# Kernel tuning notes

Hardware: AMD Instinct MI355X
Metric: run time of the kernel (lower is better)

## Reference

```python
import jax, jax.numpy as jnp
import numpy as np

B, S, H, NH = 4, 4096, 1024, 16
D = H // NH
SCALE = 1.0 / float(np.sqrt(D))


def setup_inputs() -> dict:
    key = jax.random.key(0)
    ks = jax.random.split(key, 4)
    w = 0.02
    return {
        "hidden_states": jax.random.normal(ks[0], (B, S, H), jnp.float32),
        "attention_mask": jnp.zeros((B, 1, 1, S), jnp.float32),
        "Wq": jax.random.normal(ks[1], (H, H), jnp.float32) * w,
        "bq": jnp.zeros((H,), jnp.float32),
        "Wk": jax.random.normal(ks[2], (H, H), jnp.float32) * w,
        "bk": jnp.zeros((H,), jnp.float32),
        "Wv": jax.random.normal(ks[3], (H, H), jnp.float32) * w,
        "bv": jnp.zeros((H,), jnp.float32),
    }


def reference(hidden_states, attention_mask, Wq, bq, Wk, bk, Wv, bv):
    def heads(x):  # [B,S,H] -> [B,NH,S,D]
        return x.reshape(B, S, NH, D).transpose(0, 2, 1, 3)

    q = heads(hidden_states @ Wq.T + bq)
    k = heads(hidden_states @ Wk.T + bk)
    v = heads(hidden_states @ Wv.T + bv)

    # --- global token (position 0) attends to everything ---
    gq = q[:, :, 0:1]                                   # [B,NH,1,D]
    g_scores = jnp.einsum('bhqd,bhkd->bhqk', gq, k) * SCALE + attention_mask
    g_attn = jax.nn.softmax(g_scores, axis=-1)          # [B,NH,1,S]
    g_out = jnp.einsum('bhqk,bhkd->bhqd', g_attn, v)    # [B,NH,1,D]

    # --- local tokens: 2-way attention over {own key, global key} ---
    lq = q[:, :, 1:]                                    # [B,NH,S-1,D]
    s_self = jnp.einsum('bhsd,bhsd->bhs', lq, k[:, :, 1:]) * SCALE
    s_glob = jnp.einsum('bhsd,bhd->bhs', lq, k[:, :, 0]) * SCALE
    # order matches torch cat([own, global]) along the key axis
    l_attn = jax.nn.softmax(jnp.stack([s_self, s_glob], axis=-1), axis=-1)  # [B,NH,S-1,2]
    l_out = l_attn[..., 0:1] * v[:, :, 1:] + l_attn[..., 1:2] * v[:, :, 0:1]  # [B,NH,S-1,D]

    ctx = jnp.concatenate([g_out, l_out], axis=2)       # [B,NH,S,D]
    ctx = ctx.transpose(0, 2, 1, 3).reshape(B, S, H)
    # torch returns local_attentions with shape [B,NH,S-1,1,2]
    return ctx, l_attn[:, :, :, None, :]
```

## Files before the change

### kernel.cpp

```cpp
#include <hip/hip_runtime.h>
#include <cstdint>
#include <cstddef>

#define B_   4
#define S_   4096
#define H_   1024
#define NH_  16
#define D_   64
#define M_TOT (B_ * S_)
#define K_TOT H_
#define N_TOT (3 * H_)
#define SCALE_ 0.125f
#define NCH 16
#define CH (S_ / NCH)

typedef __bf16 bf16x8 __attribute__((ext_vector_type(8)));
typedef float  f32x4  __attribute__((ext_vector_type(4)));

__device__ __forceinline__ unsigned short f2b(float x) {
    unsigned int u = __float_as_uint(x);
    u += 0x7FFFu + ((u >> 16) & 1u);
    return (unsigned short)(u >> 16);
}
__device__ __forceinline__ float b2f(unsigned int u) {
    return __uint_as_float(u << 16);
}
__device__ __forceinline__ void unp8(uint4 u, float* f) {
    f[0] = b2f(u.x & 0xffffu); f[1] = b2f(u.x >> 16);
    f[2] = b2f(u.y & 0xffffu); f[3] = b2f(u.y >> 16);
    f[4] = b2f(u.z & 0xffffu); f[5] = b2f(u.z >> 16);
    f[6] = b2f(u.w & 0xffffu); f[7] = b2f(u.w >> 16);
}
__device__ __forceinline__ unsigned int pack2(float lo, float hi) {
    return (unsigned int)f2b(lo) | ((unsigned int)f2b(hi) << 16);
}

__global__ __launch_bounds__(256) void cvt_all(const float* __restrict__ hs,
                                               const float* __restrict__ wq,
                                               const float* __restrict__ wk,
                                               const float* __restrict__ wv,
                                               unsigned short* __restrict__ Xb,
                                               unsigned short* __restrict__ Wb) {
    const int i = blockIdx.x * 256 + threadIdx.x;
    const int X8 = M_TOT * K_TOT / 8;
    const float4* sp;
    uint4* dp;
    int off;
    if (i < X8) {
        sp = (const float4*)hs;
        dp = (uint4*)Xb;
        off = i;
    } else {
        const int j = i - X8;
        const int w = j >> 17;
        off = j & 0x1ffff;
        sp = (const float4*)((w == 0) ? wq : (w == 1 ? wk : wv));
        dp = (uint4*)(Wb + (size_t)w * H_ * H_);
    }
    const float4 v0 = sp[off * 2];
    const float4 v1 = sp[off * 2 + 1];
    uint4 o;
    o.x = pack2(v0.x, v0.y);
    o.y = pack2(v0.z, v0.w);
    o.z = pack2(v1.x, v1.y);
    o.w = pack2(v1.z, v1.w);
    dp[off] = o;
}

__global__ __launch_bounds__(256) void gemm_qkv(const unsigned short* __restrict__ A,
                                                const unsigned short* __restrict__ W,
                                                const float* __restrict__ bq,
                                                const float* __restrict__ bk,
                                                const float* __restrict__ bv,
                                                unsigned short* __restrict__ C) {
    __shared__ unsigned short As[128 * 32] __attribute__((aligned(16)));
    __shared__ unsigned short Bs[128 * 32] __attribute__((aligned(16)));
    const int tid  = threadIdx.x;
    const int wid  = tid >> 6;
    const int lane = tid & 63;
    const int wm = wid >> 1, wn = wid & 1;
    const int m0 = blockIdx.y * 128;
    const int n0 = blockIdx.x * 128;

    f32x4 acc[4][4];
#pragma unroll
    for (int i = 0; i < 4; i++)
#pragma unroll
        for (int j = 0; j < 4; j++) acc[i][j] = (f32x4){0.f, 0.f, 0.f, 0.f};

    const int lrow = lane >> 2;
    const int lcol = (((lane & 3) ^ ((lrow >> 1) & 3))) * 8;

    const int rl    = lane & 15;
    const int slot8 = ((lane >> 4) ^ ((rl >> 1) & 3)) * 8;

    for (int k0 = 0; k0 < K_TOT; k0 += 32) {
#pragma unroll
        for (int i = 0; i < 2; i++) {
            const int r0 = wid * 32 + i * 16;
            const unsigned short* ga = A + (size_t)(m0 + r0 + lrow) * K_TOT + k0 + lcol;
            __builtin_amdgcn_global_load_lds(
                (const __attribute__((address_space(1))) void*)ga,
                (__attribute__((address_space(3))) void*)&As[r0 * 32], 16, 0, 0);
            const unsigned short* gb = W + (size_t)(n0 + r0 + lrow) * K_TOT + k0 + lcol;
            __builtin_amdgcn_global_load_lds(
                (const __attribute__((address_space(1))) void*)gb,
                (__attribute__((address_space(3))) void*)&Bs[r0 * 32], 16, 0, 0);
        }
        __syncthreads();

        bf16x8 af[4], bfv[4];
#pragma unroll
        for (int mi = 0; mi < 4; mi++)
            af[mi] = *(const bf16x8*)&As[(wm * 64 + mi * 16 + rl) * 32 + slot8];
#pragma unroll
        for (int ni = 0; ni < 4; ni++)
            bfv[ni] = *(const bf16x8*)&Bs[(wn * 64 + ni * 16 + rl) * 32 + slot8];
#pragma unroll
        for (int mi = 0; mi < 4; mi++)
#pragma unroll
            for (int ni = 0; ni < 4; ni++)
                acc[mi][ni] = __builtin_amdgcn_mfma_f32_16x16x32_bf16(af[mi], bfv[ni], acc[mi][ni], 0, 0, 0);
        __syncthreads();
    }

    const int col_l = lane & 15;
    const int quad  = lane >> 4;
#pragma unroll
    for (int mi = 0; mi < 4; mi++) {
#pragma unroll
        for (int ni = 0; ni < 4; ni++) {
            const int gc = n0 + wn * 64 + ni * 16 + col_l;
            const float bias = (gc < H_) ? bq[gc] : (gc < 2 * H_ ? bk[gc - H_] : bv[gc - 2 * H_]);
#pragma unroll
            for (int i = 0; i < 4; i++) {
                const int gr = m0 + wm * 64 + mi * 16 + quad * 4 + i;
                C[(size_t)gr * N_TOT + gc] = f2b(acc[mi][ni][i] + bias);
            }
        }
    }
}

__global__ __launch_bounds__(256) void gattn_part(const unsigned short* __restrict__ QKV,
                                                  const float* __restrict__ mask,
                                                  float* __restrict__ Pm,
                                                  float* __restrict__ Pl,
                                                  float* __restrict__ Po) {
    const int bh = blockIdx.x;
    const int b = bh >> 4, h = bh & 15;
    const int chunk = blockIdx.y;
    const int tid = threadIdx.x;
    const int w = tid >> 6, lane = tid & 63;

    __shared__ float gq_sh[D_];
    __shared__ float pr[CH];
    __shared__ float red[8];
    __shared__ float osum[4][D_];

    const unsigned short* gqp = QKV + (size_t)(b * S_) * N_TOT + h * D_;
    if (tid < D_) gq_sh[tid] = b2f(gqp[tid]);
    __syncthreads();

    const int s0 = chunk * CH;
    const int s  = s0 + tid;
    const uint4* kp4 = (const uint4*)(QKV + (size_t)(b * S_ + s) * N_TOT + H_ + h * D_);
    float acc = 0.f;
#pragma unroll
    for (int c = 0; c < 8; c++) {
        uint4 r = kp4[c];
        acc += b2f(r.x & 0xffffu) * gq_sh[c * 8 + 0];
        acc += b2f(r.x >> 16)     * gq_sh[c * 8 + 1];
        acc += b2f(r.y & 0xffffu) * gq_sh[c * 8 + 2];
        acc += b2f(r.y >> 16)     * gq_sh[c * 8 + 3];
        acc += b2f(r.z & 0xffffu) * gq_sh[c * 8 + 4];
        acc += b2f(r.z >> 16)     * gq_sh[c * 8 + 5];
        acc += b2f(r.w & 0xffffu) * gq_sh[c * 8 + 6];
        acc += b2f(r.w >> 16)     * gq_sh[c * 8 + 7];
    }
    const float sv = acc * SCALE_ + mask[b * S_ + s];

    float wmax = sv;
#pragma unroll
    for (int m = 32; m >= 1; m >>= 1) wmax = fmaxf(wmax, __shfl_xor(wmax, m, 64));
    if (lane == 0) red[w] = wmax;
    __syncthreads();
    const float bmax = fmaxf(fmaxf(red[0], red[1]), fmaxf(red[2], red[3]));

    const float p = __expf(sv - bmax);
    pr[tid] = p;
    float wsum = p;
#pragma unroll
    for (int m = 32; m >= 1; m >>= 1) wsum += __shfl_xor(wsum, m, 64);
    if (lane == 0) red[4 + w] = wsum;
    __syncthreads();
    const float bsum = red[4] + red[5] + red[6] + red[7];

    float o = 0.f;
    const int sbase = s0 + w * 64;
#pragma unroll 8
    for (int i = 0; i < 64; i++) {
        const int si = sbase + i;
        const float vv = b2f((unsigned int)QKV[(size_t)(b * S_ + si) * N_TOT + 2 * H_ + h * D_ + lane]);
        o += pr[w * 64 + i] * vv;
    }
    osum[w][lane] = o;
    __syncthreads();
    if (tid < D_) {
        const float ot = osum[0][tid] + osum[1][tid] + osum[2][tid] + osum[3][tid];
        Po[(size_t)(bh * NCH + chunk) * D_ + tid] = ot;
        if (tid == 0) {
            Pm[bh * NCH + chunk] = bmax;
            Pl[bh * NCH + chunk] = bsum;
        }
    }
}

__global__ __launch_bounds__(256) void lattn(const unsigned short* __restrict__ QKV,
                                             float* __restrict__ ctx,
                                             float* __restrict__ lat,
                                             const float* __restrict__ Pm,
                                             const float* __restrict__ Pl,
                                             const float* __restrict__ Po) {
    const int bh = blockIdx.x;
    const int b = bh >> 4, h = bh & 15;

    if (blockIdx.y == 128) {
        const int d = threadIdx.x;
        if (d < D_) {
            float ms = -1e30f;
#pragma unroll
            for (int c = 0; c < NCH; c++) ms = fmaxf(ms, Pm[bh * NCH + c]);
            float z = 0.f, o = 0.f;
#pragma unroll
            for (int c = 0; c < NCH; c++) {
                const float e = __expf(Pm[bh * NCH + c] - ms);
                z += Pl[bh * NCH + c] * e;
                o += Po[(size_t)(bh * NCH + c) * D_ + d] * e;
            }
            ctx[(size_t)b * S_ * H_ + (size_t)h * D_ + d] = o / z;
        }
        return;
    }

    const int w = threadIdx.x >> 6, lane = threadIdx.x & 63;
    const int g = lane >> 3;
    const int l = lane & 7;
    const int s = 1 + blockIdx.y * 32 + w * 8 + g;
    if (s >= S_) return;

    const size_t rowS = (size_t)(b * S_ + s) * N_TOT + h * D_ + l * 8;
    const size_t row0 = (size_t)(b * S_) * N_TOT + h * D_ + l * 8;

    uint4 qu  = *(const uint4*)(QKV + rowS);
    uint4 ku  = *(const uint4*)(QKV + rowS + H_);
    uint4 k0u = *(const uint4*)(QKV + row0 + H_);
    float qf[8], kf[8], k0f[8];
    unp8(qu, qf); unp8(ku, kf); unp8(k0u, k0f);

    float ps = 0.f, pg = 0.f;
#pragma unroll
    for (int i = 0; i < 8; i++) { ps += qf[i] * kf[i]; pg += qf[i] * k0f[i]; }
#pragma unroll
    for (int m = 1; m < 8; m <<= 1) {
        ps += __shfl_xor(ps, m, 64);
        pg += __shfl_xor(pg, m, 64);
    }
    ps *= SCALE_; pg *= SCALE_;
    const float mx = fmaxf(ps, pg);
    const float e0 = __expf(ps - mx), e1 = __expf(pg - mx);
    const float z = e0 + e1;
    const float p0 = e0 / z, p1 = e1 / z;

    uint4 vu  = *(const uint4*)(QKV + rowS + 2 * H_);
    uint4 v0u = *(const uint4*)(QKV + row0 + 2 * H_);
    float vf[8], v0f[8];
    unp8(vu, vf); unp8(v0u, v0f);

    float* cp = ctx + (size_t)b * (S_ * H_) + (size_t)s * H_ + h * D_ + l * 8;
    float4 o0, o1;
    o0.x = p0 * vf[0] + p1 * v0f[0];
    o0.y = p0 * vf[1] + p1 * v0f[1];
    o0.z = p0 * vf[2] + p1 * v0f[2];
    o0.w = p0 * vf[3] + p1 * v0f[3];
    o1.x = p0 * vf[4] + p1 * v0f[4];
    o1.y = p0 * vf[5] + p1 * v0f[5];
    o1.z = p0 * vf[6] + p1 * v0f[6];
    o1.w = p0 * vf[7] + p1 * v0f[7];
    ((float4*)cp)[0] = o0;
    ((float4*)cp)[1] = o1;

    if (l == 0) {
        float2 lp; lp.x = p0; lp.y = p1;
        ((float2*)(lat + ((size_t)bh * (S_ - 1) + (s - 1)) * 2))[0] = lp;
    }
}

extern "C" void kernel_launch(void* const* d_in, const int* in_sizes, int n_in,
                              void* d_out, int out_size, void* d_ws, size_t ws_size,
                              hipStream_t stream) {
    const float* hs   = (const float*)d_in[0];
    const float* mask = (const float*)d_in[1];
    const float* Wq   = (const float*)d_in[2];
    const float* bq   = (const float*)d_in[3];
    const float* Wk   = (const float*)d_in[4];
    const float* bk   = (const float*)d_in[5];
    const float* Wv   = (const float*)d_in[6];
    const float* bv   = (const float*)d_in[7];

    float* out = (float*)d_out;
    float* lat = out + (size_t)B_ * S_ * H_;

    char* ws = (char*)d_ws;
    const size_t offXb  = 0;
    const size_t offWb  = offXb  + (size_t)M_TOT * K_TOT * 2;
    const size_t offQKV = offWb  + (size_t)3 * H_ * H_ * 2;
    const size_t offPm  = offQKV + (size_t)M_TOT * N_TOT * 2;
    const size_t offPl  = offPm  + (size_t)B_ * NH_ * NCH * 4;
    const size_t offPo  = offPl  + (size_t)B_ * NH_ * NCH * 4;

    unsigned short* Xb  = (unsigned short*)(ws + offXb);
    unsigned short* Wb  = (unsigned short*)(ws + offWb);
    unsigned short* QKV = (unsigned short*)(ws + offQKV);
    float* Pm = (float*)(ws + offPm);
    float* Pl = (float*)(ws + offPl);
    float* Po = (float*)(ws + offPo);

    const int total8 = M_TOT * K_TOT / 8 + 3 * H_ * H_ / 8;
    hipLaunchKernelGGL(cvt_all, dim3(total8 / 256), dim3(256), 0, stream,
                       hs, Wq, Wk, Wv, Xb, Wb);
    hipLaunchKernelGGL(gemm_qkv, dim3(N_TOT / 128, M_TOT / 128), dim3(256), 0, stream,
                       Xb, Wb, bq, bk, bv, QKV);
    hipLaunchKernelGGL(gattn_part, dim3(B_ * NH_, NCH), dim3(256), 0, stream, QKV, mask, Pm, Pl, Po);
    hipLaunchKernelGGL(lattn, dim3(B_ * NH_, 129), dim3(256), 0, stream, QKV, out, lat, Pm, Pl, Po);
}
```

Before: 305.9 us.

## Fuse global and local attention into one kernel, deepen GEMM K-step

Merges the global-attention partial kernel and the local/combine kernel into a single launch. The global-token reduction is finalised by the last chunk block per (batch, head), tracked with an atomic counter that the conversion kernel resets. The local path is remapped so each wave covers all 16 heads of one token, giving coalesced full-row reads and writes. The QKV GEMM now stages two 32-wide K slices per barrier pair, halving the number of syncs at the cost of doubled LDS usage.

```diff
diff --git a/kernel.cpp b/kernel.cpp
--- a/kernel.cpp
+++ b/kernel.cpp
@@ -40,7 +40,9 @@
                                                const float* __restrict__ wk,
                                                const float* __restrict__ wv,
                                                unsigned short* __restrict__ Xb,
-                                               unsigned short* __restrict__ Wb) {
+                                               unsigned short* __restrict__ Wb,
+                                               int* __restrict__ cnt) {
+    if (blockIdx.x == 0 && threadIdx.x < B_ * NH_) cnt[threadIdx.x] = 0;
     const int i = blockIdx.x * 256 + threadIdx.x;
     const int X8 = M_TOT * K_TOT / 8;
     const float4* sp;
@@ -73,8 +75,8 @@
                                                 const float* __restrict__ bk,
                                                 const float* __restrict__ bv,
                                                 unsigned short* __restrict__ C) {
-    __shared__ unsigned short As[128 * 32] __attribute__((aligned(16)));
-    __shared__ unsigned short Bs[128 * 32] __attribute__((aligned(16)));
+    __shared__ unsigned short As[2][128 * 32] __attribute__((aligned(16)));
+    __shared__ unsigned short Bs[2][128 * 32] __attribute__((aligned(16)));
     const int tid  = threadIdx.x;
     const int wid  = tid >> 6;
     const int lane = tid & 63;
@@ -94,33 +96,39 @@
     const int rl    = lane & 15;
     const int slot8 = ((lane >> 4) ^ ((rl >> 1) & 3)) * 8;
 
-    for (int k0 = 0; k0 < K_TOT; k0 += 32) {
-#pragma unroll
-        for (int i = 0; i < 2; i++) {
-            const int r0 = wid * 32 + i * 16;
-            const unsigned short* ga = A + (size_t)(m0 + r0 + lrow) * K_TOT + k0 + lcol;
-            __builtin_amdgcn_global_load_lds(
-                (const __attribute__((address_space(1))) void*)ga,
-                (__attribute__((address_space(3))) void*)&As[r0 * 32], 16, 0, 0);
-            const unsigned short* gb = W + (size_t)(n0 + r0 + lrow) * K_TOT + k0 + lcol;
-            __builtin_amdgcn_global_load_lds(
-                (const __attribute__((address_space(1))) void*)gb,
-                (__attribute__((address_space(3))) void*)&Bs[r0 * 32], 16, 0, 0);
+    for (int k0 = 0; k0 < K_TOT; k0 += 64) {
+#pragma unroll
+        for (int p = 0; p < 2; p++) {
+#pragma unroll
+            for (int i = 0; i < 2; i++) {
+                const int r0 = wid * 32 + i * 16;
+                const unsigned short* ga = A + (size_t)(m0 + r0 + lrow) * K_TOT + k0 + p * 32 + lcol;
+                __builtin_amdgcn_global_load_lds(
+                    (const __attribute__((address_space(1))) void*)ga,
+                    (__attribute__((address_space(3))) void*)&As[p][r0 * 32], 16, 0, 0);
+                const unsigned short* gb = W + (size_t)(n0 + r0 + lrow) * K_TOT + k0 + p * 32 + lcol;
+                __builtin_amdgcn_global_load_lds(
+                    (const __attribute__((address_space(1))) void*)gb,
+                    (__attribute__((address_space(3))) void*)&Bs[p][r0 * 32], 16, 0, 0);
+            }
         }
         __syncthreads();
 
-        bf16x8 af[4], bfv[4];
-#pragma unroll
-        for (int mi = 0; mi < 4; mi++)
-            af[mi] = *(const bf16x8*)&As[(wm * 64 + mi * 16 + rl) * 32 + slot8];
-#pragma unroll
-        for (int ni = 0; ni < 4; ni++)
-            bfv[ni] = *(const bf16x8*)&Bs[(wn * 64 + ni * 16 + rl) * 32 + slot8];
-#pragma unroll
-        for (int mi = 0; mi < 4; mi++)
+#pragma unroll
+        for (int p = 0; p < 2; p++) {
+            bf16x8 af[4], bfv[4];
+#pragma unroll
+            for (int mi = 0; mi < 4; mi++)
+                af[mi] = *(const bf16x8*)&As[p][(wm * 64 + mi * 16 + rl) * 32 + slot8];
 #pragma unroll
             for (int ni = 0; ni < 4; ni++)
-                acc[mi][ni] = __builtin_amdgcn_mfma_f32_16x16x32_bf16(af[mi], bfv[ni], acc[mi][ni], 0, 0, 0);
+                bfv[ni] = *(const bf16x8*)&Bs[p][(wn * 64 + ni * 16 + rl) * 32 + slot8];
+#pragma unroll
+            for (int mi = 0; mi < 4; mi++)
+#pragma unroll
+                for (int ni = 0; ni < 4; ni++)
+                    acc[mi][ni] = __builtin_amdgcn_mfma_f32_16x16x32_bf16(af[mi], bfv[ni], acc[mi][ni], 0, 0, 0);
+        }
         __syncthreads();
     }
 
@@ -141,21 +149,86 @@
     }
 }
 
-__global__ __launch_bounds__(256) void gattn_part(const unsigned short* __restrict__ QKV,
-                                                  const float* __restrict__ mask,
-                                                  float* __restrict__ Pm,
-                                                  float* __restrict__ Pl,
-                                                  float* __restrict__ Po) {
-    const int bh = blockIdx.x;
+__global__ __launch_bounds__(256) void attn_all(const unsigned short* __restrict__ QKV,
+                                                const float* __restrict__ mask,
+                                                float* __restrict__ Pm,
+                                                float* __restrict__ Pl,
+                                                float* __restrict__ Po,
+                                                int* __restrict__ cnt,
+                                                float* __restrict__ ctx,
+                                                float* __restrict__ lat) {
+    const int id  = blockIdx.x;
+    const int tid = threadIdx.x;
+
+    if (id < 4096) {
+        const int b  = id >> 10;
+        const int sc = id & 1023;
+        const int w = tid >> 6, lane = tid & 63;
+        const int s = 1 + sc * 4 + w;
+        if (s >= S_) return;
+        const int h = lane >> 2, c = lane & 3;
+
+        const size_t base  = (size_t)(b * S_ + s) * N_TOT + h * D_ + c * 16;
+        const size_t base0 = (size_t)(b * S_) * N_TOT + h * D_ + c * 16;
+
+        uint4 qa = *(const uint4*)(QKV + base);
+        uint4 qb = *(const uint4*)(QKV + base + 8);
+        uint4 ka = *(const uint4*)(QKV + base + H_);
+        uint4 kb = *(const uint4*)(QKV + base + H_ + 8);
+        uint4 ga = *(const uint4*)(QKV + base0 + H_);
+        uint4 gb = *(const uint4*)(QKV + base0 + H_ + 8);
+        float qf[16], kf[16], gf[16];
+        unp8(qa, qf); unp8(qb, qf + 8);
+        unp8(ka, kf); unp8(kb, kf + 8);
+        unp8(ga, gf); unp8(gb, gf + 8);
+
+        float ps = 0.f, pg = 0.f;
+#pragma unroll
+        for (int i = 0; i < 16; i++) { ps += qf[i] * kf[i]; pg += qf[i] * gf[i]; }
+        ps += __shfl_xor(ps, 1, 64); ps += __shfl_xor(ps, 2, 64);
+        pg += __shfl_xor(pg, 1, 64); pg += __shfl_xor(pg, 2, 64);
+        ps *= SCALE_; pg *= SCALE_;
+        const float mx = fmaxf(ps, pg);
+        const float e0 = __expf(ps - mx), e1 = __expf(pg - mx);
+        const float z = e0 + e1;
+        const float p0 = e0 / z, p1 = e1 / z;
+
+        uint4 va = *(const uint4*)(QKV + base + 2 * H_);
+        uint4 vb = *(const uint4*)(QKV + base + 2 * H_ + 8);
+        uint4 ua = *(const uint4*)(QKV + base0 + 2 * H_);
+        uint4 ub = *(const uint4*)(QKV + base0 + 2 * H_ + 8);
+        float vf[16], uf[16];
+        unp8(va, vf); unp8(vb, vf + 8);
+        unp8(ua, uf); unp8(ub, uf + 8);
+
+        float* cp = ctx + (size_t)(b * S_ + s) * H_ + h * D_ + c * 16;
+#pragma unroll
+        for (int t = 0; t < 4; t++) {
+            float4 o;
+            o.x = p0 * vf[t * 4 + 0] + p1 * uf[t * 4 + 0];
+            o.y = p0 * vf[t * 4 + 1] + p1 * uf[t * 4 + 1];
+            o.z = p0 * vf[t * 4 + 2] + p1 * uf[t * 4 + 2];
+            o.w = p0 * vf[t * 4 + 3] + p1 * uf[t * 4 + 3];
+            ((float4*)cp)[t] = o;
+        }
+        if (c == 0) {
+            float2 lp; lp.x = p0; lp.y = p1;
+            ((float2*)(lat + ((size_t)(b * NH_ + h) * (S_ - 1) + (s - 1)) * 2))[0] = lp;
+        }
+        return;
+    }
+
+    const int j  = id - 4096;
+    const int bh = j >> 4;
+    const int chunk = j & 15;
     const int b = bh >> 4, h = bh & 15;
-    const int chunk = blockIdx.y;
-    const int tid = threadIdx.x;
     const int w = tid >> 6, lane = tid & 63;
 
     __shared__ float gq_sh[D_];
     __shared__ float pr[CH];
     __shared__ float red[8];
     __shared__ float osum[4][D_];
+    __shared__ int lastFlag;
 
     const unsigned short* gqp = QKV + (size_t)(b * S_) * N_TOT + h * D_;
     if (tid < D_) gq_sh[tid] = b2f(gqp[tid]);
@@ -213,85 +286,27 @@
             Pl[bh * NCH + chunk] = bsum;
         }
     }
-}
-
-__global__ __launch_bounds__(256) void lattn(const unsigned short* __restrict__ QKV,
-                                             float* __restrict__ ctx,
-                                             float* __restrict__ lat,
-                                             const float* __restrict__ Pm,
-                                             const float* __restrict__ Pl,
-                                             const float* __restrict__ Po) {
-    const int bh = blockIdx.x;
-    const int b = bh >> 4, h = bh & 15;
-
-    if (blockIdx.y == 128) {
-        const int d = threadIdx.x;
+    if (tid == 0) {
+        __threadfence();
+        lastFlag = (atomicAdd(&cnt[bh], 1) == NCH - 1);
+    }
+    __syncthreads();
+    if (lastFlag) {
+        __threadfence();
+        const int d = tid;
         if (d < D_) {
             float ms = -1e30f;
 #pragma unroll
             for (int c = 0; c < NCH; c++) ms = fmaxf(ms, Pm[bh * NCH + c]);
-            float z = 0.f, o = 0.f;
+            float z = 0.f, oo = 0.f;
 #pragma unroll
             for (int c = 0; c < NCH; c++) {
                 const float e = __expf(Pm[bh * NCH + c] - ms);
                 z += Pl[bh * NCH + c] * e;
-                o += Po[(size_t)(bh * NCH + c) * D_ + d] * e;
+                oo += Po[(size_t)(bh * NCH + c) * D_ + d] * e;
             }
-            ctx[(size_t)b * S_ * H_ + (size_t)h * D_ + d] = o / z;
-        }
-        return;
-    }
-
-    const int w = threadIdx.x >> 6, lane = threadIdx.x & 63;
-    const int g = lane >> 3;
-    const int l = lane & 7;
-    const int s = 1 + blockIdx.y * 32 + w * 8 + g;
-    if (s >= S_) return;
-
-    const size_t rowS = (size_t)(b * S_ + s) * N_TOT + h * D_ + l * 8;
-    const size_t row0 = (size_t)(b * S_) * N_TOT + h * D_ + l * 8;
-
-    uint4 qu  = *(const uint4*)(QKV + rowS);
-    uint4 ku  = *(const uint4*)(QKV + rowS + H_);
-    uint4 k0u = *(const uint4*)(QKV + row0 + H_);
-    float qf[8], kf[8], k0f[8];
-    unp8(qu, qf); unp8(ku, kf); unp8(k0u, k0f);
-
-    float ps = 0.f, pg = 0.f;
-#pragma unroll
-    for (int i = 0; i < 8; i++) { ps += qf[i] * kf[i]; pg += qf[i] * k0f[i]; }
-#pragma unroll
-    for (int m = 1; m < 8; m <<= 1) {
-        ps += __shfl_xor(ps, m, 64);
-        pg += __shfl_xor(pg, m, 64);
-    }
-    ps *= SCALE_; pg *= SCALE_;
-    const float mx = fmaxf(ps, pg);
-    const float e0 = __expf(ps - mx), e1 = __expf(pg - mx);
-    const float z = e0 + e1;
-    const float p0 = e0 / z, p1 = e1 / z;
-
-    uint4 vu  = *(const uint4*)(QKV + rowS + 2 * H_);
-    uint4 v0u = *(const uint4*)(QKV + row0 + 2 * H_);
-    float vf[8], v0f[8];
-    unp8(vu, vf); unp8(v0u, v0f);
-
-    float* cp = ctx + (size_t)b * (S_ * H_) + (size_t)s * H_ + h * D_ + l * 8;
-    float4 o0, o1;
-    o0.x = p0 * vf[0] + p1 * v0f[0];
-    o0.y = p0 * vf[1] + p1 * v0f[1];
-    o0.z = p0 * vf[2] + p1 * v0f[2];
-    o0.w = p0 * vf[3] + p1 * v0f[3];
-    o1.x = p0 * vf[4] + p1 * v0f[4];
-    o1.y = p0 * vf[5] + p1 * v0f[5];
-    o1.z = p0 * vf[6] + p1 * v0f[6];
-    o1.w = p0 * vf[7] + p1 * v0f[7];
-    ((float4*)cp)[0] = o0;
-    ((float4*)cp)[1] = o1;
-
-    if (l == 0) {
-        float2 lp; lp.x = p0; lp.y = p1;
-        ((float2*)(lat + ((size_t)bh * (S_ - 1) + (s - 1)) * 2))[0] = lp;
+            ctx[(size_t)b * S_ * H_ + (size_t)h * D_ + d] = oo / z;
+        }
     }
 }
 
@@ -317,6 +332,7 @@
     const size_t offPm  = offQKV + (size_t)M_TOT * N_TOT * 2;
     const size_t offPl  = offPm  + (size_t)B_ * NH_ * NCH * 4;
     const size_t offPo  = offPl  + (size_t)B_ * NH_ * NCH * 4;
+    const size_t offCnt = offPo  + (size_t)B_ * NH_ * NCH * D_ * 4;
 
     unsigned short* Xb  = (unsigned short*)(ws + offXb);
     unsigned short* Wb  = (unsigned short*)(ws + offWb);
@@ -324,12 +340,13 @@
     float* Pm = (float*)(ws + offPm);
     float* Pl = (float*)(ws + offPl);
     float* Po = (float*)(ws + offPo);
+    int*   cnt = (int*)(ws + offCnt);
 
     const int total8 = M_TOT * K_TOT / 8 + 3 * H_ * H_ / 8;
     hipLaunchKernelGGL(cvt_all, dim3(total8 / 256), dim3(256), 0, stream,
-                       hs, Wq, Wk, Wv, Xb, Wb);
+                       hs, Wq, Wk, Wv, Xb, Wb, cnt);
     hipLaunchKernelGGL(gemm_qkv, dim3(N_TOT / 128, M_TOT / 128), dim3(256), 0, stream,
                        Xb, Wb, bq, bk, bv, QKV);
-    hipLaunchKernelGGL(gattn_part, dim3(B_ * NH_, NCH), dim3(256), 0, stream, QKV, mask, Pm, Pl, Po);
-    hipLaunchKernelGGL(lattn, dim3(B_ * NH_, 129), dim3(256), 0, stream, QKV, out, lat, Pm, Pl, Po);
-}
+    hipLaunchKernelGGL(attn_all, dim3(4096 + B_ * NH_ * NCH), dim3(256), 0, stream,
+                       QKV, mask, Pm, Pl, Po, cnt, out, lat);
+}
```

New measurement: 344.8 us. +12.7%, slower.
